# Kernel optimization log

Measured on AMD Instinct MI355X. Metric: run time of the kernel, lower is better.

## Reference

```python
import jax, jax.numpy as jnp
import numpy as np

B, S, H, I, E = 2, 2048, 1024, 4096, 8
NUM_STEPS = 2
RMS_EPS = 1e-6


def rmsnorm(x, w, eps=RMS_EPS):
    var = jnp.mean(jnp.square(x), axis=-1, keepdims=True)
    return x * jax.lax.rsqrt(var + eps) * w


def setup_inputs() -> dict:
    key = jax.random.key(0)
    ks = jax.random.split(key, 7)
    return {
        "hidden_states": jax.random.normal(ks[0], (B, S, H), dtype=jnp.float32),
        "gate_w": jax.random.normal(ks[1], (E, H), dtype=jnp.float32) * 0.02,
        "w1": jax.random.normal(ks[2], (E, H, I), dtype=jnp.float32) * 0.02,
        "b1": jnp.zeros((E, I), dtype=jnp.float32),
        "w2": jax.random.normal(ks[3], (E, I, H), dtype=jnp.float32) * 0.02,
        "b2": jnp.zeros((E, H), dtype=jnp.float32),
        "ln_w": jnp.ones((H,), dtype=jnp.float32),
    }


def reference(hidden_states, gate_w, w1, b1, w2, b2, ln_w):
    x = hidden_states  # [B,S,H]
    dtype = hidden_states.dtype
    for i in range(NUM_STEPS):
        inp = x if i == 0 else rmsnorm(x, ln_w)
        t = inp.reshape(-1, H)  # [T,H], T = B*S
        # softmax gate (computed in fp32 as in the original)
        logits = t @ gate_w.T  # [T,E]
        rw = jax.nn.softmax(logits.astype(jnp.float32), axis=-1).astype(dtype)
        # all experts on all tokens (dense MoE), batched over E
        h = jax.nn.silu(jnp.einsum('td,edi->tei', t, w1) + b1)  # [T,E,I]
        eo = jnp.einsum('tei,eih->teh', h, w2) + b2             # [T,E,H]
        comb = jnp.einsum('te,teh->th', rw, eo)                 # weighted combine
        x = x + comb.reshape(B, S, H)
    return x  # final_projection is Identity (no feature extractor)
```

## Files before the change

### kernel.cpp

```cpp
#include <hip/hip_runtime.h>
#include <hip/hip_bf16.h>

#define T_TOK 4096
#define H_DIM 1024
#define I_DIM 4096
#define E_EXP 8
#define RMS_EPS_F 1e-6f

using bf16x8 = __attribute__((ext_vector_type(8))) __bf16;
using f32x4  = __attribute__((ext_vector_type(4))) float;

__device__ inline void gload_lds16(const void* g, void* l) {
    __builtin_amdgcn_global_load_lds(
        (const __attribute__((address_space(1))) void*)g,
        (__attribute__((address_space(3))) void*)l,
        16, 0, 0);
}

__global__ __launch_bounds__(256) void k_transpose_cvt(
    const float* __restrict__ in, __hip_bfloat16* __restrict__ out, int R, int C)
{
    __shared__ float tile[32][33];
    const size_t mat = (size_t)R * C;
    in  += (size_t)blockIdx.z * mat;
    out += (size_t)blockIdx.z * mat;
    const int c0 = blockIdx.x * 32, r0 = blockIdx.y * 32;
    const int tx = threadIdx.x & 31, ty = threadIdx.x >> 5;
#pragma unroll
    for (int dy = 0; dy < 32; dy += 8)
        tile[ty + dy][tx] = in[(size_t)(r0 + ty + dy) * C + (c0 + tx)];
    __syncthreads();
#pragma unroll
    for (int dy = 0; dy < 32; dy += 8)
        out[(size_t)(c0 + ty + dy) * R + (r0 + tx)] = __float2bfloat16(tile[tx][ty + dy]);
}

__global__ __launch_bounds__(256) void k_prep(
    const float* __restrict__ x, const float* __restrict__ lnw,
    __hip_bfloat16* __restrict__ tb, int do_norm)
{
    const int t = blockIdx.x;
    const float* row = x + (size_t)t * H_DIM;
    const int base = threadIdx.x * 4;
    float4 v = *(const float4*)(row + base);
    if (do_norm) {
        float ss = v.x*v.x + v.y*v.y + v.z*v.z + v.w*v.w;
#pragma unroll
        for (int off = 32; off > 0; off >>= 1) ss += __shfl_xor(ss, off);
        __shared__ float wsum[4];
        const int w = threadIdx.x >> 6;
        if ((threadIdx.x & 63) == 0) wsum[w] = ss;
        __syncthreads();
        const float tot = wsum[0] + wsum[1] + wsum[2] + wsum[3];
        const float scale = rsqrtf(tot * (1.0f / H_DIM) + RMS_EPS_F);
        float4 g = *(const float4*)(lnw + base);
        v.x *= scale * g.x; v.y *= scale * g.y; v.z *= scale * g.z; v.w *= scale * g.w;
    }
    __hip_bfloat16* o = tb + (size_t)t * H_DIM + base;
    o[0] = __float2bfloat16(v.x); o[1] = __float2bfloat16(v.y);
    o[2] = __float2bfloat16(v.z); o[3] = __float2bfloat16(v.w);
}

__global__ __launch_bounds__(256) void k_gate(
    const __hip_bfloat16* __restrict__ tb, const float* __restrict__ gw,
    float* __restrict__ rw)
{
    const int t = blockIdx.x * 4 + (threadIdx.x >> 6);
    const int lane = threadIdx.x & 63;
    const __hip_bfloat16* row = tb + (size_t)t * H_DIM;
    float acc[E_EXP];
#pragma unroll
    for (int e = 0; e < E_EXP; ++e) acc[e] = 0.f;
    for (int h = lane; h < H_DIM; h += 64) {
        const float xv = __bfloat162float(row[h]);
#pragma unroll
        for (int e = 0; e < E_EXP; ++e) acc[e] += xv * gw[e * H_DIM + h];
    }
#pragma unroll
    for (int e = 0; e < E_EXP; ++e) {
#pragma unroll
        for (int off = 32; off > 0; off >>= 1) acc[e] += __shfl_xor(acc[e], off);
    }
    if (lane == 0) {
        float mx = acc[0];
#pragma unroll
        for (int e = 1; e < E_EXP; ++e) mx = fmaxf(mx, acc[e]);
        float ex[E_EXP], s = 0.f;
#pragma unroll
        for (int e = 0; e < E_EXP; ++e) { ex[e] = __expf(acc[e] - mx); s += ex[e]; }
        const float inv = 1.f / s;
#pragma unroll
        for (int e = 0; e < E_EXP; ++e) rw[(size_t)t * E_EXP + e] = ex[e] * inv;
    }
}


template<int MB, int NB>
__device__ __forceinline__ void mfma_q(const bf16x8 (&a)[4][2], const bf16x8 (&b)[2][2],
                                       f32x4 (&acc)[8][4]) {
    __builtin_amdgcn_s_setprio(1);
#pragma unroll
    for (int mi = 0; mi < 4; ++mi)
#pragma unroll
        for (int nn = 0; nn < 2; ++nn)
#pragma unroll
            for (int kc = 0; kc < 2; ++kc)
                acc[MB + mi][NB + nn] = __builtin_amdgcn_mfma_f32_16x16x32_bf16(
                    a[mi][kc], b[nn][kc], acc[MB + mi][NB + nn], 0, 0, 0);
    __builtin_amdgcn_s_setprio(0);
}

template<int BB, int MBASE>
__device__ __forceinline__ void ld_a(bf16x8 (&a)[4][2], const char* rdA, int kof0, int kof1) {
#pragma unroll
    for (int mi = 0; mi < 4; ++mi) {
        a[mi][0] = *(const bf16x8*)(rdA + BB * 32768 + (MBASE + mi) * 2048 + kof0);
        a[mi][1] = *(const bf16x8*)(rdA + BB * 32768 + (MBASE + mi) * 2048 + kof1);
    }
}
template<int BB, int NBASE>
__device__ __forceinline__ void ld_b(bf16x8 (&b)[2][2], const char* rdB, int kof0, int kof1) {
#pragma unroll
    for (int ni = 0; ni < 2; ++ni) {
        b[ni][0] = *(const bf16x8*)(rdB + BB * 32768 + (NBASE + ni) * 2048 + kof0);
        b[ni][1] = *(const bf16x8*)(rdB + BB * 32768 + (NBASE + ni) * 2048 + kof1);
    }
}

#define BAR()   __builtin_amdgcn_s_barrier()
#define LGKM0() asm volatile("s_waitcnt lgkmcnt(0)" ::: "memory")
#define LGKM8() asm volatile("s_waitcnt lgkmcnt(8)" ::: "memory")
#define VMW(n)  asm volatile("s_waitcnt vmcnt(" #n ")" ::: "memory")
#define SCHED0() __builtin_amdgcn_sched_barrier(0)

template <int MODE>
__global__ __launch_bounds__(512, 2) void k_gemm8(
    const __hip_bfloat16* __restrict__ A, int lda, long long strideA,
    const __hip_bfloat16* __restrict__ Bt, int ldb, long long strideB,
    const float* __restrict__ bias, int strideBias,
    void* __restrict__ out, int ldo, long long strideOut, int K)
{
    __shared__ __hip_bfloat16 sA[2][2][128 * 64];
    __shared__ __hip_bfloat16 sB[2][2][128 * 64];

    const int z = blockIdx.z;
    A  += (size_t)z * (size_t)strideA;
    Bt += (size_t)z * (size_t)strideB;

    const int tid  = threadIdx.x;
    const int lane = tid & 63;
    const int wid  = tid >> 6;
    const int wr = wid >> 2, wc = wid & 3;
    const int m0 = blockIdx.y * 256, n0 = blockIdx.x * 256;

    const int sr  = tid >> 3;
    const int skb = ((((tid & 7) * 16) ^ ((sr & 7) << 4)) >> 1);
    const __hip_bfloat16* gA = A  + (size_t)(m0 + sr) * lda + skb;
    const __hip_bfloat16* gB = Bt + (size_t)(n0 + sr) * ldb + skb;
    char* const dA = (char*)&sA[0][0][0] + tid * 16;
    char* const dB = (char*)&sB[0][0][0] + tid * 16;

#define STAGE_A(bb, hh, kt) do { \
    const __hip_bfloat16* s_ = gA + (size_t)(hh) * 128 * lda + (size_t)(kt) * 64; \
    gload_lds16(s_,                     dA + (bb) * 32768 + (hh) * 16384); \
    gload_lds16(s_ + (size_t)64 * lda,  dA + (bb) * 32768 + (hh) * 16384 + 8192); \
} while (0)
#define STAGE_B(bb, hh, kt) do { \
    const __hip_bfloat16* s_ = gB + (size_t)(hh) * 128 * ldb + (size_t)(kt) * 64; \
    gload_lds16(s_,                     dB + (bb) * 32768 + (hh) * 16384); \
    gload_lds16(s_ + (size_t)64 * ldb,  dB + (bb) * 32768 + (hh) * 16384 + 8192); \
} while (0)

    const int fr = lane & 15, kg = lane >> 4;
    const int msk  = (fr & 7) << 4;
    const int kof0 = (kg * 16) ^ msk;
    const int kof1 = (64 + kg * 16) ^ msk;
    const char* rdA = (const char*)&sA[0][wr][0] + fr * 128;
    const char* rdB = (const char*)&sB[0][wc >> 1][0] + (wc & 1) * 8192 + fr * 128;

    f32x4  acc[8][4] = {};
    bf16x8 aL[4][2], aH[4][2], bL[2][2], bH[2][2];

    const int NT = K >> 6;

    STAGE_B(0, 0, 0); STAGE_B(0, 1, 0);
    STAGE_A(0, 0, 0); STAGE_A(0, 1, 0);
    STAGE_B(1, 0, 1); STAGE_B(1, 1, 1);
    VMW(4); BAR(); SCHED0();

    for (int i = 0; i < NT / 2 - 1; ++i) {
        const int t1 = 2 * i + 1;
        ld_a<0, 0>(aL, rdA, kof0, kof1);
        ld_b<0, 0>(bL, rdB, kof0, kof1);
        STAGE_A(1, 0, t1);
        LGKM8(); SCHED0();
        BAR(); LGKM0(); SCHED0();
        mfma_q<0, 0>(aL, bL, acc);
        BAR();
        ld_b<0, 2>(bH, rdB, kof0, kof1);
        STAGE_A(1, 1, t1);
        SCHED0();
        BAR(); LGKM0(); SCHED0();
        mfma_q<0, 2>(aL, bH, acc);
        BAR();
        ld_a<0, 4>(aH, rdA, kof0, kof1);
        STAGE_B(0, 0, t1 + 1);
        SCHED0();
        BAR(); LGKM0(); SCHED0();
        mfma_q<4, 0>(aH, bL, acc);
        BAR();
        STAGE_B(0, 1, t1 + 1);
        SCHED0();
        BAR();
        mfma_q<4, 2>(aH, bH, acc);
        VMW(4); BAR(); SCHED0();
        ld_a<1, 0>(aL, rdA, kof0, kof1);
        ld_b<1, 0>(bL, rdB, kof0, kof1);
        STAGE_A(0, 0, t1 + 1);
        LGKM8(); SCHED0();
        BAR(); LGKM0(); SCHED0();
        mfma_q<0, 0>(aL, bL, acc);
        BAR();
        ld_b<1, 2>(bH, rdB, kof0, kof1);
        STAGE_A(0, 1, t1 + 1);
        SCHED0();
        BAR(); LGKM0(); SCHED0();
        mfma_q<0, 2>(aL, bH, acc);
        BAR();
        ld_a<1, 4>(aH, rdA, kof0, kof1);
        STAGE_B(1, 0, t1 + 2);
        SCHED0();
        BAR(); LGKM0(); SCHED0();
        mfma_q<4, 0>(aH, bL, acc);
        BAR();
        STAGE_B(1, 1, t1 + 2);
        SCHED0();
        BAR();
        mfma_q<4, 2>(aH, bH, acc);
        VMW(4); BAR(); SCHED0();
    }
    {
        const int t1 = NT - 1;
        ld_a<0, 0>(aL, rdA, kof0, kof1);
        ld_b<0, 0>(bL, rdB, kof0, kof1);
        STAGE_A(1, 0, t1);
        LGKM8(); SCHED0();
        BAR(); LGKM0(); SCHED0();
        mfma_q<0, 0>(aL, bL, acc);
        BAR();
        ld_b<0, 2>(bH, rdB, kof0, kof1);
        STAGE_A(1, 1, t1);
        SCHED0();
        BAR(); LGKM0(); SCHED0();
        mfma_q<0, 2>(aL, bH, acc);
        BAR();
        ld_a<0, 4>(aH, rdA, kof0, kof1);
        SCHED0();
        BAR(); LGKM0(); SCHED0();
        mfma_q<4, 0>(aH, bL, acc);
        BAR();
        mfma_q<4, 2>(aH, bH, acc);
        VMW(0); BAR(); SCHED0();
        ld_a<1, 0>(aL, rdA, kof0, kof1);
        ld_b<1, 0>(bL, rdB, kof0, kof1);
        LGKM0(); SCHED0();
        mfma_q<0, 0>(aL, bL, acc);
        ld_b<1, 2>(bH, rdB, kof0, kof1);
        LGKM0(); SCHED0();
        mfma_q<0, 2>(aL, bH, acc);
        ld_a<1, 4>(aH, rdA, kof0, kof1);
        LGKM0(); SCHED0();
        mfma_q<4, 0>(aH, bL, acc);
        mfma_q<4, 2>(aH, bH, acc);
    }

    const int rB = kg * 4;
    if (MODE == 0) {
        __hip_bfloat16* O = (__hip_bfloat16*)out + (size_t)z * (size_t)strideOut;
        const float* bz = bias + (size_t)z * (size_t)strideBias;
#pragma unroll
        for (int mi = 0; mi < 8; ++mi) {
            const int gm = m0 + wr * 128 + mi * 16 + rB;
#pragma unroll
            for (int ni = 0; ni < 4; ++ni) {
                const int gn = n0 + wc * 64 + ni * 16 + fr;
                const float bv = bz[gn];
#pragma unroll
                for (int j = 0; j < 4; ++j) {
                    float v = acc[mi][ni][j] + bv;
                    v = v / (1.f + __expf(-v));
                    O[(size_t)(gm + j) * ldo + gn] = __float2bfloat16(v);
                }
            }
        }
    } else {
        float* O = (float*)out + (size_t)z * (size_t)strideOut;
#pragma unroll
        for (int mi = 0; mi < 8; ++mi) {
            const int gm = m0 + wr * 128 + mi * 16 + rB;
#pragma unroll
            for (int ni = 0; ni < 4; ++ni) {
                const int gn = n0 + wc * 64 + ni * 16 + fr;
#pragma unroll
                for (int j = 0; j < 4; ++j)
                    O[(size_t)(gm + j) * ldo + gn] = acc[mi][ni][j];
            }
        }
    }
#undef STAGE_A
#undef STAGE_B
}

__global__ __launch_bounds__(256) void k_combine(
    const float* __restrict__ eo, const float* __restrict__ rw,
    const float* __restrict__ b2, float* __restrict__ x, int e0, int g)
{
    const int t = blockIdx.x;
    const int h = threadIdx.x * 4;
    float4 acc = *(const float4*)(x + (size_t)t * H_DIM + h);
    for (int j = 0; j < g; ++j) {
        const float w = rw[(size_t)t * E_EXP + e0 + j];
        const float4 v  = *(const float4*)(eo + ((size_t)j * T_TOK + t) * H_DIM + h);
        const float4 bz = *(const float4*)(b2 + (size_t)(e0 + j) * H_DIM + h);
        acc.x += w * (v.x + bz.x);
        acc.y += w * (v.y + bz.y);
        acc.z += w * (v.z + bz.z);
        acc.w += w * (v.w + bz.w);
    }
    *(float4*)(x + (size_t)t * H_DIM + h) = acc;
}

extern "C" void kernel_launch(void* const* d_in, const int* in_sizes, int n_in,
                              void* d_out, int out_size, void* d_ws, size_t ws_size,
                              hipStream_t stream)
{
    const float* hidden = (const float*)d_in[0];
    const float* gate_w = (const float*)d_in[1];
    const float* w1     = (const float*)d_in[2];
    const float* b1     = (const float*)d_in[3];
    const float* w2     = (const float*)d_in[4];
    const float* b2     = (const float*)d_in[5];
    const float* ln_w   = (const float*)d_in[6];
    float* x = (float*)d_out;

    const size_t w1t_b = (size_t)E_EXP * I_DIM * H_DIM * 2;
    const size_t w2t_b = (size_t)E_EXP * H_DIM * I_DIM * 2;
    const size_t tb_b  = (size_t)T_TOK * H_DIM * 2;
    const size_t rw_b  = (size_t)T_TOK * E_EXP * 4;
    const size_t hb1_b = (size_t)T_TOK * I_DIM * 2;
    const size_t eo1_b = (size_t)T_TOK * H_DIM * 4;
    const size_t base_b = w1t_b + w2t_b + tb_b + rw_b;

    int g = 0;
    for (int cand = 8; cand >= 1; cand >>= 1)
        if (base_b + (size_t)cand * (hb1_b + eo1_b) <= ws_size) { g = cand; break; }

    char* ws = (char*)d_ws;
    __hip_bfloat16* w1t = (__hip_bfloat16*)ws;  ws += w1t_b;
    __hip_bfloat16* w2t = (__hip_bfloat16*)ws;  ws += w2t_b;
    __hip_bfloat16* tb  = (__hip_bfloat16*)ws;  ws += tb_b;
    float*          rw  = (float*)ws;           ws += rw_b;
    __hip_bfloat16* hb  = (__hip_bfloat16*)ws;
    float*          eo  = (float*)(ws + (size_t)(g > 0 ? g : 1) * hb1_b);

    hipMemcpyAsync(x, hidden, (size_t)T_TOK * H_DIM * 4, hipMemcpyDeviceToDevice, stream);

    if (g == 0) return;

    k_transpose_cvt<<<dim3(I_DIM / 32, H_DIM / 32, E_EXP), 256, 0, stream>>>(w1, w1t, H_DIM, I_DIM);
    k_transpose_cvt<<<dim3(H_DIM / 32, I_DIM / 32, E_EXP), 256, 0, stream>>>(w2, w2t, I_DIM, H_DIM);

    for (int step = 0; step < 2; ++step) {
        k_prep<<<T_TOK, 256, 0, stream>>>(x, ln_w, tb, step);
        k_gate<<<T_TOK / 4, 256, 0, stream>>>(tb, gate_w, rw);

        for (int e0 = 0; e0 < E_EXP; e0 += g) {
            k_gemm8<0><<<dim3(I_DIM / 256, T_TOK / 256, g), 512, 0, stream>>>(
                tb, H_DIM, 0,
                w1t + (size_t)e0 * I_DIM * H_DIM, H_DIM, (long long)I_DIM * H_DIM,
                b1 + (size_t)e0 * I_DIM, I_DIM,
                hb, I_DIM, (long long)T_TOK * I_DIM, H_DIM);
            k_gemm8<2><<<dim3(H_DIM / 256, T_TOK / 256, g), 512, 0, stream>>>(
                hb, I_DIM, (long long)T_TOK * I_DIM,
                w2t + (size_t)e0 * H_DIM * I_DIM, I_DIM, (long long)H_DIM * I_DIM,
                nullptr, 0,
                eo, H_DIM, (long long)T_TOK * H_DIM, I_DIM);
            k_combine<<<T_TOK, 256, 0, stream>>>(eo, rw, b2, x, e0, g);
        }
    }
}
```

Before: 1.421 ms.

## Restructure GEMM to 16 waves per 256x256 tile with 64x64 warp tiles

Changes the bf16 GEMM kernel from 8 waves (512 threads, 128x64 per wave, 2 blocks/CU) to 16 waves (1024 threads, 64x64 per wave, 1 block/CU) on the same 256x256 block tile. Each thread now issues one global->LDS load per stage and holds half the accumulators, and the main loop is rewritten as a simpler per-k-chunk macro. The aim is more latency hiding and lower register pressure per wave. In exchange, per-CU residency drops to one block, and more LDS reads are needed per MFMA, since A and B fragments are each reused across only 4 tiles.

```diff
diff --git a/kernel.cpp b/kernel.cpp
--- a/kernel.cpp
+++ b/kernel.cpp
@@ -95,46 +95,40 @@
 }
 
 
-template<int MB, int NB>
-__device__ __forceinline__ void mfma_q(const bf16x8 (&a)[4][2], const bf16x8 (&b)[2][2],
-                                       f32x4 (&acc)[8][4]) {
+template<int BB>
+__device__ __forceinline__ void ld_a4k(bf16x8 (&a)[4], const char* rdA, int kof) {
+#pragma unroll
+    for (int mi = 0; mi < 4; ++mi)
+        a[mi] = *(const bf16x8*)(rdA + BB * 32768 + mi * 2048 + kof);
+}
+template<int BB>
+__device__ __forceinline__ void ld_b42(bf16x8 (&b)[4][2], const char* rdB, int kof0, int kof1) {
+#pragma unroll
+    for (int ni = 0; ni < 4; ++ni) {
+        b[ni][0] = *(const bf16x8*)(rdB + BB * 32768 + ni * 2048 + kof0);
+        b[ni][1] = *(const bf16x8*)(rdB + BB * 32768 + ni * 2048 + kof1);
+    }
+}
+template<int KC>
+__device__ __forceinline__ void mfma16(const bf16x8 (&a)[4], const bf16x8 (&b)[4][2],
+                                       f32x4 (&acc)[4][4]) {
     __builtin_amdgcn_s_setprio(1);
 #pragma unroll
     for (int mi = 0; mi < 4; ++mi)
 #pragma unroll
-        for (int nn = 0; nn < 2; ++nn)
-#pragma unroll
-            for (int kc = 0; kc < 2; ++kc)
-                acc[MB + mi][NB + nn] = __builtin_amdgcn_mfma_f32_16x16x32_bf16(
-                    a[mi][kc], b[nn][kc], acc[MB + mi][NB + nn], 0, 0, 0);
+        for (int ni = 0; ni < 4; ++ni)
+            acc[mi][ni] = __builtin_amdgcn_mfma_f32_16x16x32_bf16(
+                a[mi], b[ni][KC], acc[mi][ni], 0, 0, 0);
     __builtin_amdgcn_s_setprio(0);
-}
-
-template<int BB, int MBASE>
-__device__ __forceinline__ void ld_a(bf16x8 (&a)[4][2], const char* rdA, int kof0, int kof1) {
-#pragma unroll
-    for (int mi = 0; mi < 4; ++mi) {
-        a[mi][0] = *(const bf16x8*)(rdA + BB * 32768 + (MBASE + mi) * 2048 + kof0);
-        a[mi][1] = *(const bf16x8*)(rdA + BB * 32768 + (MBASE + mi) * 2048 + kof1);
-    }
-}
-template<int BB, int NBASE>
-__device__ __forceinline__ void ld_b(bf16x8 (&b)[2][2], const char* rdB, int kof0, int kof1) {
-#pragma unroll
-    for (int ni = 0; ni < 2; ++ni) {
-        b[ni][0] = *(const bf16x8*)(rdB + BB * 32768 + (NBASE + ni) * 2048 + kof0);
-        b[ni][1] = *(const bf16x8*)(rdB + BB * 32768 + (NBASE + ni) * 2048 + kof1);
-    }
 }
 
 #define BAR()   __builtin_amdgcn_s_barrier()
 #define LGKM0() asm volatile("s_waitcnt lgkmcnt(0)" ::: "memory")
-#define LGKM8() asm volatile("s_waitcnt lgkmcnt(8)" ::: "memory")
 #define VMW(n)  asm volatile("s_waitcnt vmcnt(" #n ")" ::: "memory")
 #define SCHED0() __builtin_amdgcn_sched_barrier(0)
 
 template <int MODE>
-__global__ __launch_bounds__(512, 2) void k_gemm8(
+__global__ __launch_bounds__(1024, 1) void k_gemm16(
     const __hip_bfloat16* __restrict__ A, int lda, long long strideA,
     const __hip_bfloat16* __restrict__ Bt, int ldb, long long strideB,
     const float* __restrict__ bias, int strideBias,
@@ -160,118 +154,66 @@
     char* const dA = (char*)&sA[0][0][0] + tid * 16;
     char* const dB = (char*)&sB[0][0][0] + tid * 16;
 
-#define STAGE_A(bb, hh, kt) do { \
-    const __hip_bfloat16* s_ = gA + (size_t)(hh) * 128 * lda + (size_t)(kt) * 64; \
-    gload_lds16(s_,                     dA + (bb) * 32768 + (hh) * 16384); \
-    gload_lds16(s_ + (size_t)64 * lda,  dA + (bb) * 32768 + (hh) * 16384 + 8192); \
-} while (0)
-#define STAGE_B(bb, hh, kt) do { \
-    const __hip_bfloat16* s_ = gB + (size_t)(hh) * 128 * ldb + (size_t)(kt) * 64; \
-    gload_lds16(s_,                     dB + (bb) * 32768 + (hh) * 16384); \
-    gload_lds16(s_ + (size_t)64 * ldb,  dB + (bb) * 32768 + (hh) * 16384 + 8192); \
-} while (0)
+#define STAGE_A(bb, hh, kt) \
+    gload_lds16(gA + (size_t)(hh) * 128 * lda + (size_t)(kt) * 64, dA + (bb) * 32768 + (hh) * 16384)
+#define STAGE_B(bb, hh, kt) \
+    gload_lds16(gB + (size_t)(hh) * 128 * ldb + (size_t)(kt) * 64, dB + (bb) * 32768 + (hh) * 16384)
 
     const int fr = lane & 15, kg = lane >> 4;
     const int msk  = (fr & 7) << 4;
     const int kof0 = (kg * 16) ^ msk;
     const int kof1 = (64 + kg * 16) ^ msk;
-    const char* rdA = (const char*)&sA[0][wr][0] + fr * 128;
-    const char* rdB = (const char*)&sB[0][wc >> 1][0] + (wc & 1) * 8192 + fr * 128;
-
-    f32x4  acc[8][4] = {};
-    bf16x8 aL[4][2], aH[4][2], bL[2][2], bH[2][2];
+    const char* rdA = (const char*)&sA[0][0][0] + wr * 8192 + fr * 128;
+    const char* rdB = (const char*)&sB[0][0][0] + wc * 8192 + fr * 128;
+
+    f32x4  acc[4][4] = {};
+    bf16x8 a[4];
+    bf16x8 bfr[4][2];
 
     const int NT = K >> 6;
 
     STAGE_B(0, 0, 0); STAGE_B(0, 1, 0);
     STAGE_A(0, 0, 0); STAGE_A(0, 1, 0);
     STAGE_B(1, 0, 1); STAGE_B(1, 1, 1);
-    VMW(4); BAR(); SCHED0();
+    VMW(2); BAR(); SCHED0();
+
+#define TILE_STEADY(BUF, t) do { \
+    ld_b42<BUF>(bfr, rdB, kof0, kof1); \
+    ld_a4k<BUF>(a, rdA, kof0); \
+    STAGE_A(BUF ^ 1, 0, (t) + 1); STAGE_A(BUF ^ 1, 1, (t) + 1); \
+    BAR(); LGKM0(); SCHED0(); \
+    mfma16<0>(a, bfr, acc); SCHED0(); \
+    BAR(); \
+    ld_a4k<BUF>(a, rdA, kof1); \
+    STAGE_B(BUF, 0, (t) + 2); STAGE_B(BUF, 1, (t) + 2); \
+    BAR(); LGKM0(); SCHED0(); \
+    mfma16<1>(a, bfr, acc); SCHED0(); \
+    VMW(2); BAR(); SCHED0(); \
+} while (0)
 
     for (int i = 0; i < NT / 2 - 1; ++i) {
-        const int t1 = 2 * i + 1;
-        ld_a<0, 0>(aL, rdA, kof0, kof1);
-        ld_b<0, 0>(bL, rdB, kof0, kof1);
-        STAGE_A(1, 0, t1);
-        LGKM8(); SCHED0();
+        const int t0 = 2 * i;
+        TILE_STEADY(0, t0);
+        TILE_STEADY(1, t0 + 1);
+    }
+    {
+        ld_b42<0>(bfr, rdB, kof0, kof1);
+        ld_a4k<0>(a, rdA, kof0);
+        STAGE_A(1, 0, NT - 1); STAGE_A(1, 1, NT - 1);
         BAR(); LGKM0(); SCHED0();
-        mfma_q<0, 0>(aL, bL, acc);
+        mfma16<0>(a, bfr, acc); SCHED0();
         BAR();
-        ld_b<0, 2>(bH, rdB, kof0, kof1);
-        STAGE_A(1, 1, t1);
-        SCHED0();
+        ld_a4k<0>(a, rdA, kof1);
         BAR(); LGKM0(); SCHED0();
-        mfma_q<0, 2>(aL, bH, acc);
-        BAR();
-        ld_a<0, 4>(aH, rdA, kof0, kof1);
-        STAGE_B(0, 0, t1 + 1);
-        SCHED0();
-        BAR(); LGKM0(); SCHED0();
-        mfma_q<4, 0>(aH, bL, acc);
-        BAR();
-        STAGE_B(0, 1, t1 + 1);
-        SCHED0();
-        BAR();
-        mfma_q<4, 2>(aH, bH, acc);
-        VMW(4); BAR(); SCHED0();
-        ld_a<1, 0>(aL, rdA, kof0, kof1);
-        ld_b<1, 0>(bL, rdB, kof0, kof1);
-        STAGE_A(0, 0, t1 + 1);
-        LGKM8(); SCHED0();
-        BAR(); LGKM0(); SCHED0();
-        mfma_q<0, 0>(aL, bL, acc);
-        BAR();
-        ld_b<1, 2>(bH, rdB, kof0, kof1);
-        STAGE_A(0, 1, t1 + 1);
-        SCHED0();
-        BAR(); LGKM0(); SCHED0();
-        mfma_q<0, 2>(aL, bH, acc);
-        BAR();
-        ld_a<1, 4>(aH, rdA, kof0, kof1);
-        STAGE_B(1, 0, t1 + 2);
-        SCHED0();
-        BAR(); LGKM0(); SCHED0();
-        mfma_q<4, 0>(aH, bL, acc);
-        BAR();
-        STAGE_B(1, 1, t1 + 2);
-        SCHED0();
-        BAR();
-        mfma_q<4, 2>(aH, bH, acc);
-        VMW(4); BAR(); SCHED0();
-    }
-    {
-        const int t1 = NT - 1;
-        ld_a<0, 0>(aL, rdA, kof0, kof1);
-        ld_b<0, 0>(bL, rdB, kof0, kof1);
-        STAGE_A(1, 0, t1);
-        LGKM8(); SCHED0();
-        BAR(); LGKM0(); SCHED0();
-        mfma_q<0, 0>(aL, bL, acc);
-        BAR();
-        ld_b<0, 2>(bH, rdB, kof0, kof1);
-        STAGE_A(1, 1, t1);
-        SCHED0();
-        BAR(); LGKM0(); SCHED0();
-        mfma_q<0, 2>(aL, bH, acc);
-        BAR();
-        ld_a<0, 4>(aH, rdA, kof0, kof1);
-        SCHED0();
-        BAR(); LGKM0(); SCHED0();
-        mfma_q<4, 0>(aH, bL, acc);
-        BAR();
-        mfma_q<4, 2>(aH, bH, acc);
+        mfma16<1>(a, bfr, acc); SCHED0();
         VMW(0); BAR(); SCHED0();
-        ld_a<1, 0>(aL, rdA, kof0, kof1);
-        ld_b<1, 0>(bL, rdB, kof0, kof1);
+        ld_b42<1>(bfr, rdB, kof0, kof1);
+        ld_a4k<1>(a, rdA, kof0);
         LGKM0(); SCHED0();
-        mfma_q<0, 0>(aL, bL, acc);
-        ld_b<1, 2>(bH, rdB, kof0, kof1);
+        mfma16<0>(a, bfr, acc); SCHED0();
+        ld_a4k<1>(a, rdA, kof1);
         LGKM0(); SCHED0();
-        mfma_q<0, 2>(aL, bH, acc);
-        ld_a<1, 4>(aH, rdA, kof0, kof1);
-        LGKM0(); SCHED0();
-        mfma_q<4, 0>(aH, bL, acc);
-        mfma_q<4, 2>(aH, bH, acc);
+        mfma16<1>(a, bfr, acc);
     }
 
     const int rB = kg * 4;
@@ -279,8 +221,8 @@
         __hip_bfloat16* O = (__hip_bfloat16*)out + (size_t)z * (size_t)strideOut;
         const float* bz = bias + (size_t)z * (size_t)strideBias;
 #pragma unroll
-        for (int mi = 0; mi < 8; ++mi) {
-            const int gm = m0 + wr * 128 + mi * 16 + rB;
+        for (int mi = 0; mi < 4; ++mi) {
+            const int gm = m0 + wr * 64 + mi * 16 + rB;
 #pragma unroll
             for (int ni = 0; ni < 4; ++ni) {
                 const int gn = n0 + wc * 64 + ni * 16 + fr;
@@ -296,8 +238,8 @@
     } else {
         float* O = (float*)out + (size_t)z * (size_t)strideOut;
 #pragma unroll
-        for (int mi = 0; mi < 8; ++mi) {
-            const int gm = m0 + wr * 128 + mi * 16 + rB;
+        for (int mi = 0; mi < 4; ++mi) {
+            const int gm = m0 + wr * 64 + mi * 16 + rB;
 #pragma unroll
             for (int ni = 0; ni < 4; ++ni) {
                 const int gn = n0 + wc * 64 + ni * 16 + fr;
@@ -309,6 +251,7 @@
     }
 #undef STAGE_A
 #undef STAGE_B
+#undef TILE_STEADY
 }
 
 __global__ __launch_bounds__(256) void k_combine(
@@ -375,12 +318,12 @@
         k_gate<<<T_TOK / 4, 256, 0, stream>>>(tb, gate_w, rw);
 
         for (int e0 = 0; e0 < E_EXP; e0 += g) {
-            k_gemm8<0><<<dim3(I_DIM / 256, T_TOK / 256, g), 512, 0, stream>>>(
+            k_gemm16<0><<<dim3(I_DIM / 256, T_TOK / 256, g), 1024, 0, stream>>>(
                 tb, H_DIM, 0,
                 w1t + (size_t)e0 * I_DIM * H_DIM, H_DIM, (long long)I_DIM * H_DIM,
                 b1 + (size_t)e0 * I_DIM, I_DIM,
                 hb, I_DIM, (long long)T_TOK * I_DIM, H_DIM);
-            k_gemm8<2><<<dim3(H_DIM / 256, T_TOK / 256, g), 512, 0, stream>>>(
+            k_gemm16<2><<<dim3(H_DIM / 256, T_TOK / 256, g), 1024, 0, stream>>>(
                 hb, I_DIM, (long long)T_TOK * I_DIM,
                 w2t + (size_t)e0 * H_DIM * I_DIM, I_DIM, (long long)H_DIM * I_DIM,
                 nullptr, 0,
```

Result: slower. 2.175 ms (+53.0%).
